# Optimization experiments

Hardware: AMD Instinct MI355X
Metric: run time of the kernel (lower is better)

Reference implementation:

```python
import jax, jax.numpy as jnp
import numpy as np

B, I, J, DIN, DOUT = 256, 1152, 10, 8, 16
ROUTING_ITERS = 3


def squash(v):
    # v: [..., D]; squash(v) = (|v|^2 / (1+|v|^2)) * v/|v| = v * |v| / (1+|v|^2)
    l2 = jnp.linalg.norm(v, axis=-1, keepdims=True)
    return v * (l2 / (1.0 + l2 * l2))


def setup_inputs() -> dict:
    key = jax.random.key(0)
    k1, k2 = jax.random.split(key)
    x = jax.random.normal(k1, (B, I, DIN), dtype=jnp.float32)
    # per-(i,j) Linear(DIN -> DOUT, bias=False) weights, stacked: [I, J, DOUT, DIN]
    W = jax.random.normal(k2, (I, J, DOUT, DIN), dtype=jnp.float32) * 0.1
    return {"x": x, "W": W}


def reference(x, W):
    # prediction vectors u[b,i,j,:] = W[i,j] @ x[b,i,:]  -> [B, I, J, DOUT]
    u = jnp.einsum('bid,ijod->bijo', x, W)
    b = jnp.zeros((I, J), dtype=u.dtype)  # routing logits (shared across batch)
    s = None
    for _ in range(ROUTING_ITERS):
        c = jax.nn.softmax(b, axis=-1)              # [I, J]
        s = jnp.einsum('ij,bijd->bjd', c, u)        # coupling-weighted sum over in-caps
        s = squash(s)                               # [B, J, DOUT]
        # agreement: b[i,j] += sum_b <u[b,i,j], s[b,j]>
        b = b + jnp.einsum('bijd,bjd->ij', u, s)
    return s
```

## Files before the change

### kernel.cpp

```cpp
#include <hip/hip_runtime.h>
#include <math.h>

typedef unsigned short ushort_t;
typedef __attribute__((ext_vector_type(8))) __bf16 bf16x8;
typedef __attribute__((ext_vector_type(4))) float floatx4;

#define B_    256
#define I_    1152
#define J_    10
#define DIN_  8
#define DOUT_ 16
#define K_    (I_*DIN_)
#define N_    (J_*DOUT_)
#define WPS   16
#define KCHUNK (K_/WPS)
#define KSTEPS (KCHUNK/32)

static __device__ __forceinline__ ushort_t f2bf(float f) {
    unsigned int u = __float_as_uint(f);
    u += 0x7fffu + ((u >> 16) & 1u);
    return (ushort_t)(u >> 16);
}
static __device__ __forceinline__ float bf2f(ushort_t h) {
    return __uint_as_float(((unsigned int)h) << 16);
}

__global__ __launch_bounds__(1024)
void gemm_s_fused_kernel(const float* __restrict__ x, const float* __restrict__ W,
                         const float* __restrict__ blog, float* __restrict__ s_out,
                         ushort_t* __restrict__ Sbt_hi, ushort_t* __restrict__ Sbt_lo,
                         const int iter)
{
    const int tid  = threadIdx.x;
    const int blk  = blockIdx.x;
    const int xcd  = blk & 7;
    const int sl   = blk >> 3;
    const int mb   = (xcd >> 1) * 4 + (sl & 3);
    const int nt   = (xcd & 1) * 5 + (sl >> 2);
    const int lane = tid & 63;
    const int w    = tid >> 6;

    __shared__ float   c_lds[I_];
    __shared__ floatx4 part[WPS * 64];

    if (iter > 0) {
        for (int r2 = tid; r2 < I_; r2 += 1024) {
            const float* br = blog + (size_t)r2 * J_;
            float bv[J_];
            float mx = -1e30f;
            #pragma unroll
            for (int j = 0; j < J_; ++j) { bv[j] = br[j]; mx = fmaxf(mx, bv[j]); }
            float sum = 0.f;
            #pragma unroll
            for (int j = 0; j < J_; ++j) { bv[j] = __expf(bv[j] - mx); sum += bv[j]; }
            c_lds[r2] = bv[nt] / sum;
        }
        __syncthreads();
    }

    {
        const int r = lane & 15, q = lane >> 4;
        const float* ap = x + (size_t)(mb * 16 + r) * K_ + w * KCHUNK + 8 * q;
        const float* wp = W + (((size_t)(w * 72 + q) * J_ + nt) * DOUT_ + r) * DIN_;
        const size_t wstep = (size_t)4 * J_ * DOUT_ * DIN_;
        floatx4 acc = {0.f, 0.f, 0.f, 0.f};

        float4 xa0 = *(const float4*)(ap);
        float4 xa1 = *(const float4*)(ap + 4);
        float4 w0  = *(const float4*)(wp);
        float4 w1  = *(const float4*)(wp + 4);
        #pragma unroll
        for (int s = 0; s < KSTEPS; ++s) {
            float4 nxa0, nxa1, nw0, nw1;
            if (s + 1 < KSTEPS) {
                nxa0 = *(const float4*)(ap + (s + 1) * 32);
                nxa1 = *(const float4*)(ap + (s + 1) * 32 + 4);
                nw0  = *(const float4*)(wp + (s + 1) * wstep);
                nw1  = *(const float4*)(wp + (s + 1) * wstep + 4);
            }
            float cs   = (iter == 0) ? 0.1f : c_lds[w * 72 + 4 * s + q];
            float xv[8]  = {xa0.x, xa0.y, xa0.z, xa0.w, xa1.x, xa1.y, xa1.z, xa1.w};
            float wvv[8] = {w0.x, w0.y, w0.z, w0.w, w1.x, w1.y, w1.z, w1.w};
            bf16x8 ah, al, bh, bl;
            #pragma unroll
            for (int e = 0; e < 8; ++e) {
                float xe = xv[e];
                __bf16 h = (__bf16)xe;
                ah[e] = h;
                al[e] = (__bf16)(xe - (float)h);
                float pe = wvv[e] * cs;
                __bf16 g = (__bf16)pe;
                bh[e] = g;
                bl[e] = (__bf16)(pe - (float)g);
            }
            acc = __builtin_amdgcn_mfma_f32_16x16x32_bf16(ah, bh, acc, 0, 0, 0);
            acc = __builtin_amdgcn_mfma_f32_16x16x32_bf16(al, bh, acc, 0, 0, 0);
            acc = __builtin_amdgcn_mfma_f32_16x16x32_bf16(ah, bl, acc, 0, 0, 0);
            if (s + 1 < KSTEPS) { xa0 = nxa0; xa1 = nxa1; w0 = nw0; w1 = nw1; }
        }
        part[w * 64 + lane] = acc;
    }
    __syncthreads();

    if (tid < 256) {
        const int b_local = tid >> 4;
        const int o       = tid & 15;
        const int lane_c  = ((b_local >> 2) << 4) | o;
        const int reg     = b_local & 3;
        float v = 0.f;
        #pragma unroll
        for (int u = 0; u < WPS; ++u)
            v += part[u * 64 + lane_c][reg];
        float sq = v * v;
        #pragma unroll
        for (int off = 1; off < 16; off <<= 1)
            sq += __shfl_xor(sq, off, 16);
        float l2 = sqrtf(sq);
        float val = v * (l2 / (1.f + sq));
        const int b  = mb * 16 + b_local;
        const int jo = nt * 16 + o;
        if (iter == 2) {
            s_out[(size_t)b * N_ + jo] = val;
        } else {
            ushort_t hi = f2bf(val);
            Sbt_hi[(size_t)jo * B_ + b] = hi;
            Sbt_lo[(size_t)jo * B_ + b] = f2bf(val - bf2f(hi));
        }
    }
}

__global__ __launch_bounds__(256)
void gemm_bupd_kernel(const float* __restrict__ x,
                      const ushort_t* __restrict__ Sbt_hi, const ushort_t* __restrict__ Sbt_lo,
                      const float* __restrict__ W, float* __restrict__ blog,
                      const int first)
{
    int wv   = blockIdx.x * 4 + (threadIdx.x >> 6);
    int lane = threadIdx.x & 63;
    int mt = wv / 5;
    int jp = wv - mt * 5;
    int j0 = jp * 2, j1 = jp * 2 + 1;
    int r = lane & 15, q = lane >> 4;
    const float* xp = x + (size_t)(8 * q) * K_ + (mt * 16 + r);
    size_t b0off = (size_t)(j0 * 16 + r) * B_ + 8 * q;
    size_t b1off = (size_t)(j1 * 16 + r) * B_ + 8 * q;
    floatx4 acc0 = {0.f, 0.f, 0.f, 0.f};
    floatx4 acc1 = {0.f, 0.f, 0.f, 0.f};

    float xcur[8], xnxt[8];
    #pragma unroll
    for (int e = 0; e < 8; ++e) xcur[e] = xp[(size_t)e * K_];
    #pragma unroll
    for (int s = 0; s < B_ / 32; ++s) {
        if (s + 1 < B_ / 32) {
            #pragma unroll
            for (int e = 0; e < 8; ++e)
                xnxt[e] = xp[(size_t)((s + 1) * 32 + e) * K_];
        }
        bf16x8 ah, al;
        #pragma unroll
        for (int e = 0; e < 8; ++e) {
            float v = xcur[e];
            __bf16 h = (__bf16)v;
            ah[e] = h;
            al[e] = (__bf16)(v - (float)h);
        }
        bf16x8 bh0 = *(const bf16x8*)(Sbt_hi + b0off + s * 32);
        bf16x8 bl0 = *(const bf16x8*)(Sbt_lo + b0off + s * 32);
        bf16x8 bh1 = *(const bf16x8*)(Sbt_hi + b1off + s * 32);
        bf16x8 bl1 = *(const bf16x8*)(Sbt_lo + b1off + s * 32);
        acc0 = __builtin_amdgcn_mfma_f32_16x16x32_bf16(ah, bh0, acc0, 0, 0, 0);
        acc0 = __builtin_amdgcn_mfma_f32_16x16x32_bf16(al, bh0, acc0, 0, 0, 0);
        acc0 = __builtin_amdgcn_mfma_f32_16x16x32_bf16(ah, bl0, acc0, 0, 0, 0);
        acc1 = __builtin_amdgcn_mfma_f32_16x16x32_bf16(ah, bh1, acc1, 0, 0, 0);
        acc1 = __builtin_amdgcn_mfma_f32_16x16x32_bf16(al, bh1, acc1, 0, 0, 0);
        acc1 = __builtin_amdgcn_mfma_f32_16x16x32_bf16(ah, bl1, acc1, 0, 0, 0);
        #pragma unroll
        for (int e = 0; e < 8; ++e) xcur[e] = xnxt[e];
    }
    int i  = mt * 2 + (q >> 1);
    int d0 = (q & 1) * 4;
    int o  = lane & 15;
    int iw = mt * 2 + (lane >> 5);
    {
        const float4 w4 = *(const float4*)(W + ((((size_t)i * J_ + j0) * DOUT_ + o) * DIN_ + d0));
        float val = acc0[0] * w4.x + acc0[1] * w4.y + acc0[2] * w4.z + acc0[3] * w4.w;
        #pragma unroll
        for (int off = 1; off < 32; off <<= 1)
            val += __shfl_xor(val, off, 32);
        if ((lane & 31) == 0) {
            float* dst = blog + (size_t)iw * J_ + j0;
            if (first) *dst = val; else *dst += val;
        }
    }
    {
        const float4 w4 = *(const float4*)(W + ((((size_t)i * J_ + j1) * DOUT_ + o) * DIN_ + d0));
        float val = acc1[0] * w4.x + acc1[1] * w4.y + acc1[2] * w4.z + acc1[3] * w4.w;
        #pragma unroll
        for (int off = 1; off < 32; off <<= 1)
            val += __shfl_xor(val, off, 32);
        if ((lane & 31) == 0) {
            float* dst = blog + (size_t)iw * J_ + j1;
            if (first) *dst = val; else *dst += val;
        }
    }
}

extern "C" void kernel_launch(void* const* d_in, const int* in_sizes, int n_in,
                              void* d_out, int out_size, void* d_ws, size_t ws_size,
                              hipStream_t stream)
{
    const float* x = (const float*)d_in[0];
    const float* W = (const float*)d_in[1];
    float* s_out = (float*)d_out;

    char* ws = (char*)d_ws;
    ushort_t* Sbt_hi = (ushort_t*)(ws);
    ushort_t* Sbt_lo = (ushort_t*)(ws + 81920);
    float*    blog   = (float*)   (ws + 163840);

    for (int it = 0; it < 3; ++it) {
        gemm_s_fused_kernel<<<160, 1024, 0, stream>>>(x, W, blog, s_out,
                                                      Sbt_hi, Sbt_lo, it);
        if (it < 2)
            gemm_bupd_kernel<<<720, 256, 0, stream>>>(x, Sbt_hi, Sbt_lo,
                                                      W, blog, it == 0 ? 1 : 0);
    }
}
```

Before: 160.8 us.

## Split s-GEMM across 1280 small blocks with atomic cross-block K reduction

The fused s kernel changes from 160 blocks of 1024 threads to 1280 blocks of 128 threads. The K dimension is split across 8 blocks per output tile, each block adds its partial sums into a global accumulator with atomics, and the last arriving block (found via a counter) applies the squash and writes the result. This is meant to spread the work over more CUs. The softmax is computed only for each block's slice of rows, the loads are double-buffered two steps ahead, and the bupd kernel's block-to-wave mapping is remapped by XCD. In exchange it adds a memset, global atomics, thread fences and a counter protocol that relies on the counts from earlier iterations.

```diff
diff --git a/kernel.cpp b/kernel.cpp
--- a/kernel.cpp
+++ b/kernel.cpp
@@ -12,8 +12,8 @@
 #define DOUT_ 16
 #define K_    (I_*DIN_)
 #define N_    (J_*DOUT_)
-#define WPS   16
-#define KCHUNK (K_/WPS)
+#define KSPLIT 16
+#define KCHUNK (K_/KSPLIT)
 #define KSTEPS (KCHUNK/32)
 
 static __device__ __forceinline__ ushort_t f2bf(float f) {
@@ -25,27 +25,30 @@
     return __uint_as_float(((unsigned int)h) << 16);
 }
 
-__global__ __launch_bounds__(1024)
+__global__ __launch_bounds__(128)
 void gemm_s_fused_kernel(const float* __restrict__ x, const float* __restrict__ W,
                          const float* __restrict__ blog, float* __restrict__ s_out,
                          ushort_t* __restrict__ Sbt_hi, ushort_t* __restrict__ Sbt_lo,
+                         float* __restrict__ s_accum, unsigned int* __restrict__ cnt,
                          const int iter)
 {
     const int tid  = threadIdx.x;
     const int blk  = blockIdx.x;
-    const int xcd  = blk & 7;
-    const int sl   = blk >> 3;
-    const int mb   = (xcd >> 1) * 4 + (sl & 3);
-    const int nt   = (xcd & 1) * 5 + (sl >> 2);
+    const int kb   = blk & 7;
+    const int tile = blk >> 3;
+    const int mb   = tile & 15;
+    const int nt   = tile >> 4;
     const int lane = tid & 63;
     const int w    = tid >> 6;
-
-    __shared__ float   c_lds[I_];
-    __shared__ floatx4 part[WPS * 64];
+    const int kc   = kb * 2 + w;
+
+    __shared__ float   c_lds[144];
+    __shared__ floatx4 part[2 * 64];
+    __shared__ int     last_s;
 
     if (iter > 0) {
-        for (int r2 = tid; r2 < I_; r2 += 1024) {
-            const float* br = blog + (size_t)r2 * J_;
+        for (int r2 = tid; r2 < 144; r2 += 128) {
+            const float* br = blog + (size_t)(kb * 144 + r2) * J_;
             float bv[J_];
             float mx = -1e30f;
             #pragma unroll
@@ -60,25 +63,30 @@
 
     {
         const int r = lane & 15, q = lane >> 4;
-        const float* ap = x + (size_t)(mb * 16 + r) * K_ + w * KCHUNK + 8 * q;
-        const float* wp = W + (((size_t)(w * 72 + q) * J_ + nt) * DOUT_ + r) * DIN_;
+        const float* ap = x + (size_t)(mb * 16 + r) * K_ + kc * KCHUNK + 8 * q;
+        const float* wp = W + (((size_t)(kc * 72 + q) * J_ + nt) * DOUT_ + r) * DIN_;
         const size_t wstep = (size_t)4 * J_ * DOUT_ * DIN_;
         floatx4 acc = {0.f, 0.f, 0.f, 0.f};
 
-        float4 xa0 = *(const float4*)(ap);
-        float4 xa1 = *(const float4*)(ap + 4);
-        float4 w0  = *(const float4*)(wp);
-        float4 w1  = *(const float4*)(wp + 4);
+        float4 bxa0[2], bxa1[2], bw0[2], bw1[2];
+        #pragma unroll
+        for (int s = 0; s < 2; ++s) {
+            bxa0[s] = *(const float4*)(ap + s * 32);
+            bxa1[s] = *(const float4*)(ap + s * 32 + 4);
+            bw0[s]  = *(const float4*)(wp + s * wstep);
+            bw1[s]  = *(const float4*)(wp + s * wstep + 4);
+        }
         #pragma unroll
         for (int s = 0; s < KSTEPS; ++s) {
-            float4 nxa0, nxa1, nw0, nw1;
-            if (s + 1 < KSTEPS) {
-                nxa0 = *(const float4*)(ap + (s + 1) * 32);
-                nxa1 = *(const float4*)(ap + (s + 1) * 32 + 4);
-                nw0  = *(const float4*)(wp + (s + 1) * wstep);
-                nw1  = *(const float4*)(wp + (s + 1) * wstep + 4);
+            float4 xa0 = bxa0[s & 1], xa1 = bxa1[s & 1];
+            float4 w0  = bw0[s & 1],  w1  = bw1[s & 1];
+            if (s + 2 < KSTEPS) {
+                bxa0[s & 1] = *(const float4*)(ap + (s + 2) * 32);
+                bxa1[s & 1] = *(const float4*)(ap + (s + 2) * 32 + 4);
+                bw0[s & 1]  = *(const float4*)(wp + (s + 2) * wstep);
+                bw1[s & 1]  = *(const float4*)(wp + (s + 2) * wstep + 4);
             }
-            float cs   = (iter == 0) ? 0.1f : c_lds[w * 72 + 4 * s + q];
+            float cs = (iter == 0) ? 0.1f : c_lds[w * 72 + 4 * s + q];
             float xv[8]  = {xa0.x, xa0.y, xa0.z, xa0.w, xa1.x, xa1.y, xa1.z, xa1.w};
             float wvv[8] = {w0.x, w0.y, w0.z, w0.w, w1.x, w1.y, w1.z, w1.w};
             bf16x8 ah, al, bh, bl;
@@ -96,35 +104,54 @@
             acc = __builtin_amdgcn_mfma_f32_16x16x32_bf16(ah, bh, acc, 0, 0, 0);
             acc = __builtin_amdgcn_mfma_f32_16x16x32_bf16(al, bh, acc, 0, 0, 0);
             acc = __builtin_amdgcn_mfma_f32_16x16x32_bf16(ah, bl, acc, 0, 0, 0);
-            if (s + 1 < KSTEPS) { xa0 = nxa0; xa1 = nxa1; w0 = nw0; w1 = nw1; }
         }
         part[w * 64 + lane] = acc;
     }
     __syncthreads();
 
-    if (tid < 256) {
-        const int b_local = tid >> 4;
-        const int o       = tid & 15;
-        const int lane_c  = ((b_local >> 2) << 4) | o;
-        const int reg     = b_local & 3;
-        float v = 0.f;
-        #pragma unroll
-        for (int u = 0; u < WPS; ++u)
-            v += part[u * 64 + lane_c][reg];
-        float sq = v * v;
-        #pragma unroll
-        for (int off = 1; off < 16; off <<= 1)
-            sq += __shfl_xor(sq, off, 16);
-        float l2 = sqrtf(sq);
-        float val = v * (l2 / (1.f + sq));
-        const int b  = mb * 16 + b_local;
-        const int jo = nt * 16 + o;
+    const int row  = tid >> 3;
+    const int col2 = (tid & 7) * 2;
+    #pragma unroll
+    for (int h = 0; h < 2; ++h) {
+        const int o      = col2 + h;
+        const int lane_c = ((row >> 2) << 4) | o;
+        const int reg    = row & 3;
+        float v = part[lane_c][reg] + part[64 + lane_c][reg];
+        atomicAdd(&s_accum[tile * 256 + row * 16 + o], v);
+    }
+    __syncthreads();
+    if (tid == 0) {
+        __threadfence();
+        unsigned int old = atomicAdd(&cnt[tile], 1u);
+        last_s = (old == (unsigned int)(iter * 8 + 7));
+    }
+    __syncthreads();
+    if (!last_s) return;
+
+    __threadfence();
+    float v[2];
+    #pragma unroll
+    for (int h = 0; h < 2; ++h)
+        v[h] = __hip_atomic_load(&s_accum[tile * 256 + row * 16 + col2 + h],
+                                 __ATOMIC_RELAXED, __HIP_MEMORY_SCOPE_AGENT);
+    float sq = v[0] * v[0] + v[1] * v[1];
+    #pragma unroll
+    for (int off = 1; off < 8; off <<= 1)
+        sq += __shfl_xor(sq, off, 8);
+    float l2 = sqrtf(sq);
+    float scale = l2 / (1.f + sq);
+    const int b = mb * 16 + row;
+    #pragma unroll
+    for (int h = 0; h < 2; ++h) {
+        float val = v[h] * scale;
+        const int jo = nt * 16 + col2 + h;
         if (iter == 2) {
             s_out[(size_t)b * N_ + jo] = val;
         } else {
             ushort_t hi = f2bf(val);
             Sbt_hi[(size_t)jo * B_ + b] = hi;
             Sbt_lo[(size_t)jo * B_ + b] = f2bf(val - bf2f(hi));
+            s_accum[tile * 256 + row * 16 + col2 + h] = 0.f;
         }
     }
 }
@@ -135,7 +162,7 @@
                       const float* __restrict__ W, float* __restrict__ blog,
                       const int first)
 {
-    int wv   = blockIdx.x * 4 + (threadIdx.x >> 6);
+    int wv   = (blockIdx.x & 7) * 360 + (blockIdx.x >> 3) * 4 + (threadIdx.x >> 6);
     int lane = threadIdx.x & 63;
     int mt = wv / 5;
     int jp = wv - mt * 5;
@@ -215,13 +242,18 @@
     float* s_out = (float*)d_out;
 
     char* ws = (char*)d_ws;
-    ushort_t* Sbt_hi = (ushort_t*)(ws);
-    ushort_t* Sbt_lo = (ushort_t*)(ws + 81920);
-    float*    blog   = (float*)   (ws + 163840);
+    ushort_t*     Sbt_hi  = (ushort_t*)(ws);
+    ushort_t*     Sbt_lo  = (ushort_t*)(ws + 81920);
+    float*        blog    = (float*)   (ws + 163840);
+    float*        s_accum = (float*)   (ws + 209920);
+    unsigned int* cnt     = (unsigned int*)(ws + 373760);
+
+    (void)hipMemsetAsync(ws + 209920, 0, 164480, stream);
 
     for (int it = 0; it < 3; ++it) {
-        gemm_s_fused_kernel<<<160, 1024, 0, stream>>>(x, W, blog, s_out,
-                                                      Sbt_hi, Sbt_lo, it);
+        gemm_s_fused_kernel<<<1280, 128, 0, stream>>>(x, W, blog, s_out,
+                                                      Sbt_hi, Sbt_lo,
+                                                      s_accum, cnt, it);
         if (it < 2)
             gemm_bupd_kernel<<<720, 256, 0, stream>>>(x, Sbt_hi, Sbt_lo,
                                                       W, blog, it == 0 ? 1 : 0);
```

New measurement: 299.8 us. 1.86x slower.

## Precompute bf16 hi/lo splits of x and c-scaled W in separate prep kernels

Applied to the files above, without the earlier changes.

Adds a one-time prep kernel that splits x into bf16 hi/lo arrays and a per-iteration prep kernel that computes the softmax coupling and writes c*W as bf16 hi/lo. The main GEMM then loads pre-split bf16 operands with a two-deep register prefetch, so it no longer converts fp32 to bf16 in its inner loop or runs the softmax redundantly in every block. The b-update kernel's block-to-wave mapping is also remapped so that each XCD handles a contiguous range of tiles. The cost is four extra kernel launches and extra global traffic to write and reread the split arrays.

```diff
diff --git a/kernel.cpp b/kernel.cpp
--- a/kernel.cpp
+++ b/kernel.cpp
@@ -3,6 +3,7 @@
 
 typedef unsigned short ushort_t;
 typedef __attribute__((ext_vector_type(8))) __bf16 bf16x8;
+typedef __attribute__((ext_vector_type(4))) __bf16 bf16x4;
 typedef __attribute__((ext_vector_type(4))) float floatx4;
 
 #define B_    256
@@ -25,11 +26,82 @@
     return __uint_as_float(((unsigned int)h) << 16);
 }
 
+__global__ __launch_bounds__(256)
+void prep_x_kernel(const float* __restrict__ x,
+                   __bf16* __restrict__ xh, __bf16* __restrict__ xl)
+{
+    const int idx = blockIdx.x * 256 + threadIdx.x;
+    #pragma unroll
+    for (int t = 0; t < 4; ++t) {
+        const int i4 = idx + t * (576 * 256);
+        float4 v = *(const float4*)(x + (size_t)i4 * 4);
+        float vv[4] = {v.x, v.y, v.z, v.w};
+        bf16x4 h4, l4;
+        #pragma unroll
+        for (int e = 0; e < 4; ++e) {
+            __bf16 h = (__bf16)vv[e];
+            h4[e] = h;
+            l4[e] = (__bf16)(vv[e] - (float)h);
+        }
+        *(bf16x4*)(xh + (size_t)i4 * 4) = h4;
+        *(bf16x4*)(xl + (size_t)i4 * 4) = l4;
+    }
+}
+
+__global__ __launch_bounds__(512)
+void prep_cw_kernel(const float* __restrict__ W, const float* __restrict__ blog,
+                    __bf16* __restrict__ cwh, __bf16* __restrict__ cwl,
+                    const int iter)
+{
+    __shared__ float c_lds[160];
+    const int blk = blockIdx.x;
+    const int tid = threadIdx.x;
+
+    if (tid < 160) {
+        if (iter == 0) {
+            c_lds[tid] = 0.1f;
+        } else {
+            const int il = tid / 10, jj = tid % 10;
+            const float* br = blog + (size_t)(blk * 16 + il) * J_;
+            float bv[J_];
+            float mx = -1e30f;
+            #pragma unroll
+            for (int j = 0; j < J_; ++j) { bv[j] = br[j]; mx = fmaxf(mx, bv[j]); }
+            float sum = 0.f;
+            #pragma unroll
+            for (int j = 0; j < J_; ++j) { bv[j] = __expf(bv[j] - mx); sum += bv[j]; }
+            c_lds[tid] = bv[jj] / sum;
+        }
+    }
+    __syncthreads();
+
+    const size_t base = (size_t)blk * 20480;
+    #pragma unroll
+    for (int t = 0; t < 10; ++t) {
+        const int f4  = tid + t * 512;
+        const int loc = f4 * 4;
+        const float cs = c_lds[loc >> 7];
+        const size_t e = base + (size_t)loc;
+        float4 w4 = *(const float4*)(W + e);
+        float pv[4] = {w4.x * cs, w4.y * cs, w4.z * cs, w4.w * cs};
+        bf16x4 h4, l4;
+        #pragma unroll
+        for (int q = 0; q < 4; ++q) {
+            __bf16 h = (__bf16)pv[q];
+            h4[q] = h;
+            l4[q] = (__bf16)(pv[q] - (float)h);
+        }
+        *(bf16x4*)(cwh + e) = h4;
+        *(bf16x4*)(cwl + e) = l4;
+    }
+}
+
 __global__ __launch_bounds__(1024)
-void gemm_s_fused_kernel(const float* __restrict__ x, const float* __restrict__ W,
-                         const float* __restrict__ blog, float* __restrict__ s_out,
-                         ushort_t* __restrict__ Sbt_hi, ushort_t* __restrict__ Sbt_lo,
-                         const int iter)
+void gemm_s_kernel(const __bf16* __restrict__ xh, const __bf16* __restrict__ xl,
+                   const __bf16* __restrict__ cwh, const __bf16* __restrict__ cwl,
+                   float* __restrict__ s_out,
+                   ushort_t* __restrict__ Sbt_hi, ushort_t* __restrict__ Sbt_lo,
+                   const int iter)
 {
     const int tid  = threadIdx.x;
     const int blk  = blockIdx.x;
@@ -40,63 +112,40 @@
     const int lane = tid & 63;
     const int w    = tid >> 6;
 
-    __shared__ float   c_lds[I_];
     __shared__ floatx4 part[WPS * 64];
-
-    if (iter > 0) {
-        for (int r2 = tid; r2 < I_; r2 += 1024) {
-            const float* br = blog + (size_t)r2 * J_;
-            float bv[J_];
-            float mx = -1e30f;
-            #pragma unroll
-            for (int j = 0; j < J_; ++j) { bv[j] = br[j]; mx = fmaxf(mx, bv[j]); }
-            float sum = 0.f;
-            #pragma unroll
-            for (int j = 0; j < J_; ++j) { bv[j] = __expf(bv[j] - mx); sum += bv[j]; }
-            c_lds[r2] = bv[nt] / sum;
-        }
-        __syncthreads();
-    }
 
     {
         const int r = lane & 15, q = lane >> 4;
-        const float* ap = x + (size_t)(mb * 16 + r) * K_ + w * KCHUNK + 8 * q;
-        const float* wp = W + (((size_t)(w * 72 + q) * J_ + nt) * DOUT_ + r) * DIN_;
+        const size_t aoff = (size_t)(mb * 16 + r) * K_ + w * KCHUNK + 8 * q;
+        const __bf16* aph = xh + aoff;
+        const __bf16* apl = xl + aoff;
+        const size_t boff = (((size_t)(w * 72 + q) * J_ + nt) * DOUT_ + r) * DIN_;
+        const __bf16* wph = cwh + boff;
+        const __bf16* wpl = cwl + boff;
         const size_t wstep = (size_t)4 * J_ * DOUT_ * DIN_;
         floatx4 acc = {0.f, 0.f, 0.f, 0.f};
 
-        float4 xa0 = *(const float4*)(ap);
-        float4 xa1 = *(const float4*)(ap + 4);
-        float4 w0  = *(const float4*)(wp);
-        float4 w1  = *(const float4*)(wp + 4);
+        bf16x8 rah[2], ral[2], rbh[2], rbl[2];
+        #pragma unroll
+        for (int s = 0; s < 2; ++s) {
+            rah[s] = *(const bf16x8*)(aph + s * 32);
+            ral[s] = *(const bf16x8*)(apl + s * 32);
+            rbh[s] = *(const bf16x8*)(wph + s * wstep);
+            rbl[s] = *(const bf16x8*)(wpl + s * wstep);
+        }
         #pragma unroll
         for (int s = 0; s < KSTEPS; ++s) {
-            float4 nxa0, nxa1, nw0, nw1;
-            if (s + 1 < KSTEPS) {
-                nxa0 = *(const float4*)(ap + (s + 1) * 32);
-                nxa1 = *(const float4*)(ap + (s + 1) * 32 + 4);
-                nw0  = *(const float4*)(wp + (s + 1) * wstep);
-                nw1  = *(const float4*)(wp + (s + 1) * wstep + 4);
-            }
-            float cs   = (iter == 0) ? 0.1f : c_lds[w * 72 + 4 * s + q];
-            float xv[8]  = {xa0.x, xa0.y, xa0.z, xa0.w, xa1.x, xa1.y, xa1.z, xa1.w};
-            float wvv[8] = {w0.x, w0.y, w0.z, w0.w, w1.x, w1.y, w1.z, w1.w};
-            bf16x8 ah, al, bh, bl;
-            #pragma unroll
-            for (int e = 0; e < 8; ++e) {
-                float xe = xv[e];
-                __bf16 h = (__bf16)xe;
-                ah[e] = h;
-                al[e] = (__bf16)(xe - (float)h);
-                float pe = wvv[e] * cs;
-                __bf16 g = (__bf16)pe;
-                bh[e] = g;
-                bl[e] = (__bf16)(pe - (float)g);
+            bf16x8 ah = rah[s & 1], al = ral[s & 1];
+            bf16x8 bh = rbh[s & 1], bl = rbl[s & 1];
+            if (s + 2 < KSTEPS) {
+                rah[s & 1] = *(const bf16x8*)(aph + (s + 2) * 32);
+                ral[s & 1] = *(const bf16x8*)(apl + (s + 2) * 32);
+                rbh[s & 1] = *(const bf16x8*)(wph + (s + 2) * wstep);
+                rbl[s & 1] = *(const bf16x8*)(wpl + (s + 2) * wstep);
             }
             acc = __builtin_amdgcn_mfma_f32_16x16x32_bf16(ah, bh, acc, 0, 0, 0);
             acc = __builtin_amdgcn_mfma_f32_16x16x32_bf16(al, bh, acc, 0, 0, 0);
             acc = __builtin_amdgcn_mfma_f32_16x16x32_bf16(ah, bl, acc, 0, 0, 0);
-            if (s + 1 < KSTEPS) { xa0 = nxa0; xa1 = nxa1; w0 = nw0; w1 = nw1; }
         }
         part[w * 64 + lane] = acc;
     }
@@ -135,7 +184,7 @@
                       const float* __restrict__ W, float* __restrict__ blog,
                       const int first)
 {
-    int wv   = blockIdx.x * 4 + (threadIdx.x >> 6);
+    int wv   = (blockIdx.x & 7) * 360 + (blockIdx.x >> 3) * 4 + (threadIdx.x >> 6);
     int lane = threadIdx.x & 63;
     int mt = wv / 5;
     int jp = wv - mt * 5;
@@ -218,10 +267,16 @@
     ushort_t* Sbt_hi = (ushort_t*)(ws);
     ushort_t* Sbt_lo = (ushort_t*)(ws + 81920);
     float*    blog   = (float*)   (ws + 163840);
-
+    __bf16*   xh     = (__bf16*)  (ws + 262144);
+    __bf16*   xl     = (__bf16*)  (ws + 262144 + 4718592);
+    __bf16*   cwh    = (__bf16*)  (ws + 9699328);
+    __bf16*   cwl    = (__bf16*)  (ws + 12648448);
+
+    prep_x_kernel<<<576, 256, 0, stream>>>(x, xh, xl);
     for (int it = 0; it < 3; ++it) {
-        gemm_s_fused_kernel<<<160, 1024, 0, stream>>>(x, W, blog, s_out,
-                                                      Sbt_hi, Sbt_lo, it);
+        prep_cw_kernel<<<72, 512, 0, stream>>>(W, blog, cwh, cwl, it);
+        gemm_s_kernel<<<160, 1024, 0, stream>>>(xh, xl, cwh, cwl, s_out,
+                                                Sbt_hi, Sbt_lo, it);
         if (it < 2)
             gemm_bupd_kernel<<<720, 256, 0, stream>>>(x, Sbt_hi, Sbt_lo,
                                                       W, blog, it == 0 ? 1 : 0);
```

Measured after the change: 176.0 us. 9.4% more time.

## Prepack x into bf16 hi/lo and W into MFMA-ordered layout for routing GEMMs

Applied to the files above, without the earlier changes.

A new first kernel splits x into bf16 hi/lo parts and reorders W into a lane-contiguous packed layout stored in workspace. In the same launch it runs the iteration-0 GEMM. Later s-GEMM iterations read the packed buffers with coalesced loads and double-buffered prefetch, and skip the per-iteration x splitting. The b-update kernel also remaps its block index across XCDs. This costs extra workspace and an added packing pass, and the packing blocks share a launch with the GEMM blocks.

```diff
diff --git a/kernel.cpp b/kernel.cpp
--- a/kernel.cpp
+++ b/kernel.cpp
@@ -15,6 +15,7 @@
 #define WPS   16
 #define KCHUNK (K_/WPS)
 #define KSTEPS (KCHUNK/32)
+#define CHUNK16 2368
 
 static __device__ __forceinline__ ushort_t f2bf(float f) {
     unsigned int u = __float_as_uint(f);
@@ -26,37 +27,63 @@
 }
 
 __global__ __launch_bounds__(1024)
-void gemm_s_fused_kernel(const float* __restrict__ x, const float* __restrict__ W,
-                         const float* __restrict__ blog, float* __restrict__ s_out,
-                         ushort_t* __restrict__ Sbt_hi, ushort_t* __restrict__ Sbt_lo,
-                         const int iter)
+void prep_and_gemm0_kernel(const float* __restrict__ x, const float* __restrict__ W,
+                           ushort_t* __restrict__ xPk, float* __restrict__ wPk,
+                           ushort_t* __restrict__ Sbt_hi, ushort_t* __restrict__ Sbt_lo)
 {
-    const int tid  = threadIdx.x;
-    const int blk  = blockIdx.x;
-    const int xcd  = blk & 7;
-    const int sl   = blk >> 3;
+    const int blk = blockIdx.x;
+    const int tid = threadIdx.x;
+
+    __shared__ floatx4 part[WPS * 64];
+
+    if (blk < 288) {
+        const int gid = blk * 1024 + tid;
+        const int f   = gid * 8;
+        const int row = f / K_;
+        const int kk  = f - row * K_;
+        const int kc  = kk / KCHUNK;
+        const int t   = kk - kc * KCHUNK;
+        const int s   = t >> 5;
+        const int q   = (t & 31) >> 3;
+        const int mb  = row >> 4, r = row & 15;
+
+        const float* src = x + (size_t)f;
+        bf16x8 h8, l8;
+        #pragma unroll
+        for (int e = 0; e < 8; ++e) {
+            float v = src[e];
+            __bf16 h = (__bf16)v;
+            h8[e] = h;
+            l8[e] = (__bf16)(v - (float)h);
+        }
+        bf16x8* dst = (bf16x8*)xPk + (size_t)(mb * 16 + kc) * CHUNK16 + s * 128 + q * 16 + r;
+        dst[0]  = h8;
+        dst[64] = l8;
+        return;
+    }
+    if (blk < 648) {
+        const int gid = (blk - 288) * 1024 + tid;
+        const int f   = gid * 4;
+        const int i   = f / 1280;
+        const int rem = f - i * 1280;
+        const int no  = rem >> 3;
+        const int p   = (rem >> 2) & 1;
+        const int nt  = no >> 4, r = no & 15;
+        const int kc  = i / 72;
+        const int m   = i - kc * 72;
+        const int s   = m >> 2, q = m & 3;
+        float4 v = *(const float4*)(W + (size_t)f);
+        ((float4*)wPk)[(size_t)(nt * 16 + kc) * CHUNK16 + (s * 2 + p) * 64 + q * 16 + r] = v;
+        return;
+    }
+
+    const int blk_ = blk - 648;
+    const int xcd  = blk_ & 7;
+    const int sl   = blk_ >> 3;
     const int mb   = (xcd >> 1) * 4 + (sl & 3);
     const int nt   = (xcd & 1) * 5 + (sl >> 2);
     const int lane = tid & 63;
     const int w    = tid >> 6;
-
-    __shared__ float   c_lds[I_];
-    __shared__ floatx4 part[WPS * 64];
-
-    if (iter > 0) {
-        for (int r2 = tid; r2 < I_; r2 += 1024) {
-            const float* br = blog + (size_t)r2 * J_;
-            float bv[J_];
-            float mx = -1e30f;
-            #pragma unroll
-            for (int j = 0; j < J_; ++j) { bv[j] = br[j]; mx = fmaxf(mx, bv[j]); }
-            float sum = 0.f;
-            #pragma unroll
-            for (int j = 0; j < J_; ++j) { bv[j] = __expf(bv[j] - mx); sum += bv[j]; }
-            c_lds[r2] = bv[nt] / sum;
-        }
-        __syncthreads();
-    }
 
     {
         const int r = lane & 15, q = lane >> 4;
@@ -78,7 +105,7 @@
                 nw0  = *(const float4*)(wp + (s + 1) * wstep);
                 nw1  = *(const float4*)(wp + (s + 1) * wstep + 4);
             }
-            float cs   = (iter == 0) ? 0.1f : c_lds[w * 72 + 4 * s + q];
+            const float cs = 0.1f;
             float xv[8]  = {xa0.x, xa0.y, xa0.z, xa0.w, xa1.x, xa1.y, xa1.z, xa1.w};
             float wvv[8] = {w0.x, w0.y, w0.z, w0.w, w1.x, w1.y, w1.z, w1.w};
             bf16x8 ah, al, bh, bl;
@@ -119,6 +146,105 @@
         float val = v * (l2 / (1.f + sq));
         const int b  = mb * 16 + b_local;
         const int jo = nt * 16 + o;
+        ushort_t hi = f2bf(val);
+        Sbt_hi[(size_t)jo * B_ + b] = hi;
+        Sbt_lo[(size_t)jo * B_ + b] = f2bf(val - bf2f(hi));
+    }
+}
+
+__global__ __launch_bounds__(1024)
+void gemm_s_fused_pk_kernel(const ushort_t* __restrict__ xPk, const float* __restrict__ wPk,
+                            const float* __restrict__ blog, float* __restrict__ s_out,
+                            ushort_t* __restrict__ Sbt_hi, ushort_t* __restrict__ Sbt_lo,
+                            const int iter)
+{
+    const int tid  = threadIdx.x;
+    const int blk  = blockIdx.x;
+    const int xcd  = blk & 7;
+    const int sl   = blk >> 3;
+    const int mb   = (xcd >> 1) * 4 + (sl & 3);
+    const int nt   = (xcd & 1) * 5 + (sl >> 2);
+    const int lane = tid & 63;
+    const int w    = tid >> 6;
+
+    __shared__ float   c_lds[I_];
+    __shared__ floatx4 part[WPS * 64];
+
+    {
+        for (int r2 = tid; r2 < I_; r2 += 1024) {
+            const float* br = blog + (size_t)r2 * J_;
+            float bv[J_];
+            float mx = -1e30f;
+            #pragma unroll
+            for (int j = 0; j < J_; ++j) { bv[j] = br[j]; mx = fmaxf(mx, bv[j]); }
+            float sum = 0.f;
+            #pragma unroll
+            for (int j = 0; j < J_; ++j) { bv[j] = __expf(bv[j] - mx); sum += bv[j]; }
+            c_lds[r2] = bv[nt] / sum;
+        }
+        __syncthreads();
+    }
+
+    {
+        const int q = lane >> 4;
+        const bf16x8* xp = (const bf16x8*)xPk + (size_t)(mb * 16 + w) * CHUNK16 + lane;
+        const float4* wp = (const float4*)wPk + (size_t)(nt * 16 + w) * CHUNK16 + lane;
+        floatx4 acc = {0.f, 0.f, 0.f, 0.f};
+
+        bf16x8 rah[2], ral[2];
+        float4 rw0[2], rw1[2];
+        #pragma unroll
+        for (int s = 0; s < 2; ++s) {
+            rah[s] = xp[s * 128];
+            ral[s] = xp[s * 128 + 64];
+            rw0[s] = wp[s * 128];
+            rw1[s] = wp[s * 128 + 64];
+        }
+        #pragma unroll
+        for (int s = 0; s < KSTEPS; ++s) {
+            bf16x8 ah = rah[s & 1], al = ral[s & 1];
+            float4 w0 = rw0[s & 1], w1 = rw1[s & 1];
+            if (s + 2 < KSTEPS) {
+                rah[s & 1] = xp[(s + 2) * 128];
+                ral[s & 1] = xp[(s + 2) * 128 + 64];
+                rw0[s & 1] = wp[(s + 2) * 128];
+                rw1[s & 1] = wp[(s + 2) * 128 + 64];
+            }
+            float cs = c_lds[w * 72 + 4 * s + q];
+            float wvv[8] = {w0.x, w0.y, w0.z, w0.w, w1.x, w1.y, w1.z, w1.w};
+            bf16x8 bh, bl;
+            #pragma unroll
+            for (int e = 0; e < 8; ++e) {
+                float pe = wvv[e] * cs;
+                __bf16 g = (__bf16)pe;
+                bh[e] = g;
+                bl[e] = (__bf16)(pe - (float)g);
+            }
+            acc = __builtin_amdgcn_mfma_f32_16x16x32_bf16(ah, bh, acc, 0, 0, 0);
+            acc = __builtin_amdgcn_mfma_f32_16x16x32_bf16(al, bh, acc, 0, 0, 0);
+            acc = __builtin_amdgcn_mfma_f32_16x16x32_bf16(ah, bl, acc, 0, 0, 0);
+        }
+        part[w * 64 + lane] = acc;
+    }
+    __syncthreads();
+
+    if (tid < 256) {
+        const int b_local = tid >> 4;
+        const int o       = tid & 15;
+        const int lane_c  = ((b_local >> 2) << 4) | o;
+        const int reg     = b_local & 3;
+        float v = 0.f;
+        #pragma unroll
+        for (int u = 0; u < WPS; ++u)
+            v += part[u * 64 + lane_c][reg];
+        float sq = v * v;
+        #pragma unroll
+        for (int off = 1; off < 16; off <<= 1)
+            sq += __shfl_xor(sq, off, 16);
+        float l2 = sqrtf(sq);
+        float val = v * (l2 / (1.f + sq));
+        const int b  = mb * 16 + b_local;
+        const int jo = nt * 16 + o;
         if (iter == 2) {
             s_out[(size_t)b * N_ + jo] = val;
         } else {
@@ -135,7 +261,7 @@
                       const float* __restrict__ W, float* __restrict__ blog,
                       const int first)
 {
-    int wv   = blockIdx.x * 4 + (threadIdx.x >> 6);
+    int wv   = (blockIdx.x & 7) * 360 + (blockIdx.x >> 3) * 4 + (threadIdx.x >> 6);
     int lane = threadIdx.x & 63;
     int mt = wv / 5;
     int jp = wv - mt * 5;
@@ -218,12 +344,15 @@
     ushort_t* Sbt_hi = (ushort_t*)(ws);
     ushort_t* Sbt_lo = (ushort_t*)(ws + 81920);
     float*    blog   = (float*)   (ws + 163840);
-
-    for (int it = 0; it < 3; ++it) {
-        gemm_s_fused_kernel<<<160, 1024, 0, stream>>>(x, W, blog, s_out,
-                                                      Sbt_hi, Sbt_lo, it);
-        if (it < 2)
-            gemm_bupd_kernel<<<720, 256, 0, stream>>>(x, Sbt_hi, Sbt_lo,
-                                                      W, blog, it == 0 ? 1 : 0);
-    }
-}
+    ushort_t* xPk    = (ushort_t*)(ws + 262144);
+    float*    wPk    = (float*)   (ws + 9961472);
+
+    prep_and_gemm0_kernel<<<808, 1024, 0, stream>>>(x, W, xPk, wPk,
+                                                    Sbt_hi, Sbt_lo);
+    gemm_bupd_kernel<<<720, 256, 0, stream>>>(x, Sbt_hi, Sbt_lo, W, blog, 1);
+    gemm_s_fused_pk_kernel<<<160, 1024, 0, stream>>>(xPk, wPk, blog, s_out,
+                                                     Sbt_hi, Sbt_lo, 1);
+    gemm_bupd_kernel<<<720, 256, 0, stream>>>(x, Sbt_hi, Sbt_lo, W, blog, 0);
+    gemm_s_fused_pk_kernel<<<160, 1024, 0, stream>>>(xPk, wPk, blog, s_out,
+                                                     Sbt_hi, Sbt_lo, 2);
+}
```

Measured after the change: 169.7 us. 5.5% more time.
